# Kernel tuning notes

Hardware: AMD Instinct MI355X
Metric: run time of the kernel (lower is better)

Reference implementation:

```python
import jax, jax.numpy as jnp
import numpy as np

N_HEADS = 16
N_KV_HEADS = 4
HEAD_DIM = 64
ROPE_BASE = 10000.0

def _rope_cos_sin(T, dtype):
    # flash-attn style: cos/sin of shape [T, head_dim//2]
    inv_freq = 1.0 / (ROPE_BASE ** (jnp.arange(0, HEAD_DIM, 2, dtype=jnp.float32) / HEAD_DIM))
    freqs = jnp.arange(T, dtype=jnp.float32)[:, None] * inv_freq[None, :]  # [T, D/2]
    return jnp.cos(freqs).astype(dtype), jnp.sin(freqs).astype(dtype)

def _apply_rope(x, cos, sin):
    # x: [B, H, T, D], non-interleaved rotate-half on full head dim
    d2 = HEAD_DIM // 2
    x1, x2 = x[..., :d2], x[..., d2:]
    c = cos[None, None, :, :]
    s = sin[None, None, :, :]
    return jnp.concatenate([x1 * c - x2 * s, x2 * c + x1 * s], axis=-1)

def setup_inputs() -> dict:
    key = jax.random.key(0)
    ks = jax.random.split(key, 6)
    B, T, D = 1, 4096, 1024
    def g(k, shape, scale):
        return jax.random.normal(k, shape, dtype=jnp.float32) * scale
    return {
        "query": g(ks[0], (B, T, D), 1.0),
        "Wq": g(ks[1], (D, D), D ** -0.5),
        "Wk": g(ks[2], (D, N_KV_HEADS * HEAD_DIM), D ** -0.5),
        "Wv": g(ks[3], (D, N_KV_HEADS * HEAD_DIM), D ** -0.5),
        "W1": g(ks[4], (D, 4 * D), D ** -0.5),
        "W2": g(ks[5], (4 * D, D), (4 * D) ** -0.5),
    }

def reference(query, Wq, Wk, Wv, W1, W2):
    B, T, D = query.shape
    # QKV projections -> [B, H, T, Dh]
    q = (query @ Wq).reshape(B, T, N_HEADS, HEAD_DIM).transpose(0, 2, 1, 3)
    k = (query @ Wk).reshape(B, T, N_KV_HEADS, HEAD_DIM).transpose(0, 2, 1, 3)
    v = (query @ Wv).reshape(B, T, N_KV_HEADS, HEAD_DIM).transpose(0, 2, 1, 3)
    # RoPE (seqlen_offset = 0, no cache)
    cos, sin = _rope_cos_sin(T, q.dtype)
    q = _apply_rope(q, cos, sin)
    k = _apply_rope(k, cos, sin)
    # GQA: repeat KV heads to match Q heads
    n_rep = N_HEADS // N_KV_HEADS
    k = jnp.repeat(k, n_rep, axis=1)
    v = jnp.repeat(v, n_rep, axis=1)
    # Scaled dot-product attention, causal
    scale = HEAD_DIM ** -0.5
    scores = jnp.einsum("bhqd,bhkd->bhqk", q, k) * scale
    i = jnp.arange(T)[:, None]
    j = jnp.arange(T)[None, :]
    scores = jnp.where(j > i, jnp.finfo(scores.dtype).min, scores)
    attn = jax.nn.softmax(scores, axis=-1)
    out = jnp.einsum("bhqk,bhkd->bhqd", attn, v)  # [B, H, T, Dh]
    out = out.transpose(0, 2, 1, 3).reshape(B, T, D)
    # out_proj: Linear -> SiLU -> Linear (use_swiglu=True path)
    return jax.nn.silu(out @ W1) @ W2
```

## Files before the change

### kernel.cpp

```cpp
#include <hip/hip_runtime.h>
#include <stdint.h>

typedef unsigned short u16;
typedef __bf16 bf16x8 __attribute__((ext_vector_type(8)));
typedef float f32x4 __attribute__((ext_vector_type(4)));

#define T_SEQ 4096
#define DMODEL 1024

__device__ __forceinline__ float bf2f(u16 x) {
  union { uint32_t u; float f; } v; v.u = ((uint32_t)x) << 16; return v.f;
}
__device__ __forceinline__ u16 f2bf(float f) {
  union { float f; uint32_t u; } v; v.f = f;
  return (u16)((v.u + 0x7FFFu + ((v.u >> 16) & 1u)) >> 16);
}
__device__ __forceinline__ float fexp2(float x) {
#if __has_builtin(__builtin_amdgcn_exp2f)
  return __builtin_amdgcn_exp2f(x);
#else
  return __expf(x * 0.6931471805599453f);
#endif
}
__device__ __forceinline__ uint32_t pack_bf16(float lo, float hi) {
#if __has_builtin(__builtin_amdgcn_cvt_pk_bf16_f32)
  typedef __bf16 bf16x2_t __attribute__((ext_vector_type(2)));
  union { bf16x2_t v; uint32_t u; } c;
  c.v = __builtin_amdgcn_cvt_pk_bf16_f32(lo, hi);
  return c.u;
#else
  union { float f; uint32_t u; } a, b;
  a.f = lo; b.f = hi;
  return __builtin_amdgcn_perm(b.u + 0x8000u, a.u + 0x8000u, 0x07060302u);
#endif
}
__device__ __forceinline__ void async16(void* lds, const void* g) {
  __builtin_amdgcn_global_load_lds(
      (__attribute__((address_space(1))) void*)const_cast<void*>(g),
      (__attribute__((address_space(3))) void*)lds, 16, 0, 0);
}
__device__ __forceinline__ void storeC(u16* C, size_t i, float v) { C[i] = f2bf(v); }
__device__ __forceinline__ void storeC(float* C, size_t i, float v) { C[i] = v; }

__device__ __forceinline__ void wtrans_body(const float* __restrict__ in,
                                            u16* __restrict__ out, int K, int N,
                                            int bx, int by, int tid,
                                            float (*tile)[65]) {
  const int n0 = bx * 64, k0 = by * 64;
  const int r = tid >> 2, c = (tid & 3) * 16;
#pragma unroll
  for (int j = 0; j < 4; ++j) {
    float4 v = *(const float4*)&in[(size_t)(k0 + r) * N + n0 + c + j * 4];
    tile[r][c + j * 4 + 0] = v.x; tile[r][c + j * 4 + 1] = v.y;
    tile[r][c + j * 4 + 2] = v.z; tile[r][c + j * 4 + 3] = v.w;
  }
  __syncthreads();
  union { u16 s[16]; uint4 q[2]; } buf;
#pragma unroll
  for (int j = 0; j < 16; ++j) buf.s[j] = f2bf(tile[c + j][r]);
  u16* dst = out + (size_t)(n0 + r) * K + k0 + c;
  *(uint4*)(dst) = buf.q[0];
  *(uint4*)(dst + 8) = buf.q[1];
}

__global__ void __launch_bounds__(256) prep(const float* __restrict__ query,
                                            const float* __restrict__ Wq,
                                            const float* __restrict__ Wk,
                                            const float* __restrict__ Wv,
                                            const float* __restrict__ W1,
                                            const float* __restrict__ W2,
                                            u16* __restrict__ Xb,
                                            u16* __restrict__ WqkvT,
                                            u16* __restrict__ W1T,
                                            u16* __restrict__ W2T) {
  __shared__ float tile[64][65];
  const int b = blockIdx.x, tid = threadIdx.x;
  if (b < 4096) {
    int idx = (b * 256 + tid) * 4;
    float4 v = *(const float4*)(query + idx);
    union { u16 s[4]; uint2 q; } o;
    o.s[0] = f2bf(v.x); o.s[1] = f2bf(v.y); o.s[2] = f2bf(v.z); o.s[3] = f2bf(v.w);
    *(uint2*)(Xb + idx) = o.q;
  } else if (b < 4352) {
    int t = b - 4096;
    wtrans_body(Wq, WqkvT, 1024, 1024, t & 15, t >> 4, tid, tile);
  } else if (b < 4416) {
    int t = b - 4352;
    wtrans_body(Wk, WqkvT + (size_t)1024 * 1024, 1024, 256, t & 3, t >> 2, tid, tile);
  } else if (b < 4480) {
    int t = b - 4416;
    wtrans_body(Wv, WqkvT + (size_t)1280 * 1024, 1024, 256, t & 3, t >> 2, tid, tile);
  } else if (b < 5504) {
    int t = b - 4480;
    wtrans_body(W1, W1T, 1024, 4096, t & 63, t >> 6, tid, tile);
  } else {
    int t = b - 5504;
    wtrans_body(W2, W2T, 4096, 1024, t & 15, t >> 4, tid, tile);
  }
}

__global__ void __launch_bounds__(256) rope_vt(const u16* __restrict__ qkv,
                                               u16* __restrict__ Q,
                                               u16* __restrict__ Ko,
                                               u16* __restrict__ Vt) {
  __shared__ u16 tile[64][65];
  const int b = blockIdx.x, tid = threadIdx.x;
  if (b < 4096) {
    const int t = b;
    const int i = tid & 31;
    const float ang = (float)t * powf(10000.f, -(float)i * (1.f / 32.f));
    float s, c;
    sincosf(ang, &s, &c);
    const u16* row = qkv + (size_t)t * 1536;
    const float QS = 0.125f * 1.4426950408889634f;
    const float cq = c * QS, sq = s * QS;
#pragma unroll
    for (int it = 0; it < 2; ++it) {
      int h = (tid >> 5) + it * 8;
      float x1 = bf2f(row[h * 64 + i]);
      float x2 = bf2f(row[h * 64 + 32 + i]);
      size_t o = ((size_t)h * T_SEQ + t) * 64 + i;
      Q[o] = f2bf(x1 * cq - x2 * sq);
      Q[o + 32] = f2bf(x2 * cq + x1 * sq);
    }
    if (tid < 128) {
      int h = tid >> 5;
      float x1 = bf2f(row[1024 + h * 64 + i]);
      float x2 = bf2f(row[1024 + h * 64 + 32 + i]);
      size_t o = ((size_t)h * T_SEQ + t) * 64 + i;
      Ko[o] = f2bf(x1 * c - x2 * s);
      Ko[o + 32] = f2bf(x2 * c + x1 * s);
    }
  } else {
    const int t = b - 4096;
    const int t0 = (t & 63) * 64, h = t >> 6;
    const int r = tid >> 2, q4 = (tid & 3) * 16;
    const u16* src = qkv + (size_t)(t0 + r) * 1536 + 1280 + h * 64 + q4;
    union { u16 s[16]; uint4 q[2]; } buf;
    buf.q[0] = *(const uint4*)(src);
    buf.q[1] = *(const uint4*)(src + 8);
#pragma unroll
    for (int j = 0; j < 16; ++j) tile[r][q4 + j] = buf.s[j];
    __syncthreads();
#pragma unroll
    for (int j = 0; j < 16; ++j) buf.s[j] = tile[q4 + j][r];
    u16* dst = Vt + ((size_t)h * 64 + r) * T_SEQ + t0 + q4;
    *(uint4*)(dst) = buf.q[0];
    *(uint4*)(dst + 8) = buf.q[1];
  }
}

template <int AM, int ACT, typename OutT>
__global__ void __launch_bounds__(256) gemm_bt(const u16* __restrict__ A,
                                               const u16* __restrict__ Bt,
                                               OutT* __restrict__ C,
                                               int M, int N, int K) {
  __shared__ u16 sA[2][AM * 32][64];
  __shared__ u16 sB[2][128][64];
  const int tid = threadIdx.x;
  const int w = tid >> 6, lane = tid & 63;
  const int g = lane >> 4, l15 = lane & 15;
  const int r8 = lane >> 3, c8 = lane & 7;
  const int bm = blockIdx.y * (AM * 32), bn = blockIdx.x * 128;

  f32x4 acc[AM][4];
#pragma unroll
  for (int i = 0; i < AM; ++i)
#pragma unroll
    for (int j = 0; j < 4; ++j) acc[i][j] = (f32x4){0.f, 0.f, 0.f, 0.f};

  const u16* Ag = A + (size_t)(bm + w * (AM * 8) + r8) * K + (c8 ^ r8) * 8;
  const u16* Bg = Bt + (size_t)(bn + w * 32 + r8) * K + (c8 ^ r8) * 8;
  const int mrow = (w >> 1) * (AM * 16), ncol = (w & 1) * 64;
  const int swz = l15 & 7;

#define GSTAGE(K0, BUF)                                                        \
  {                                                                            \
    _Pragma("unroll") for (int t = 0; t < AM; ++t)                             \
      async16(&sA[BUF][w * (AM * 8) + t * 8][0], Ag + (size_t)(t * 8) * K + (K0)); \
    _Pragma("unroll") for (int t = 0; t < 4; ++t)                              \
      async16(&sB[BUF][w * 32 + t * 8][0], Bg + (size_t)(t * 8) * K + (K0));   \
  }

  GSTAGE(0, 0);
  int cur = 0;
  for (int k0 = 0; k0 < K; k0 += 64) {
    __syncthreads();
    if (k0 + 64 < K) GSTAGE(k0 + 64, cur ^ 1);
#pragma unroll
    for (int kk = 0; kk < 2; ++kk) {
      const int cb = ((kk * 4 + g) ^ swz) * 8;
      bf16x8 a[AM], b[4];
#pragma unroll
      for (int i = 0; i < AM; ++i) a[i] = *(const bf16x8*)&sA[cur][mrow + i * 16 + l15][cb];
#pragma unroll
      for (int i = 0; i < 4; ++i) b[i] = *(const bf16x8*)&sB[cur][ncol + i * 16 + l15][cb];
#pragma unroll
      for (int mi = 0; mi < AM; ++mi)
#pragma unroll
        for (int ni = 0; ni < 4; ++ni)
          acc[mi][ni] = __builtin_amdgcn_mfma_f32_16x16x32_bf16(a[mi], b[ni], acc[mi][ni], 0, 0, 0);
    }
    cur ^= 1;
  }
#undef GSTAGE
#pragma unroll
  for (int mi = 0; mi < AM; ++mi)
#pragma unroll
    for (int ni = 0; ni < 4; ++ni)
#pragma unroll
      for (int r = 0; r < 4; ++r) {
        int row = bm + mrow + mi * 16 + g * 4 + r;
        int col = bn + ncol + ni * 16 + l15;
        float v = acc[mi][ni][r];
        if (ACT == 1) v = v / (1.f + __expf(-v));
        storeC(C, (size_t)row * N + col, v);
      }
}

__global__ void __launch_bounds__(512, 2) gemm_ffn1(const u16* __restrict__ A,
                                                    const u16* __restrict__ Bt,
                                                    u16* __restrict__ C) {
  const int N = 4096, K = 1024;
  __shared__ u16 sA[2][256][64];
  __shared__ u16 sB[2][256][64];
  const int tid = threadIdx.x;
  const int w = tid >> 6, lane = tid & 63;
  const int g = lane >> 4, l15 = lane & 15;
  const int r8 = lane >> 3, c8 = lane & 7;
  const int wm = w >> 2, wn = w & 3;
  const int bm = blockIdx.y * 256, bn = blockIdx.x * 256;

  f32x4 acc[8][4];
#pragma unroll
  for (int i = 0; i < 8; ++i)
#pragma unroll
    for (int j = 0; j < 4; ++j) acc[i][j] = (f32x4){0.f, 0.f, 0.f, 0.f};

  const u16* Ag = A + (size_t)(bm + w * 32 + r8) * K + (c8 ^ r8) * 8;
  const u16* Bg = Bt + (size_t)(bn + w * 32 + r8) * K + (c8 ^ r8) * 8;
  const int mrow = wm * 128, ncol = wn * 64;
  const int swz = l15 & 7;

#define FSTAGE(K0, BUF)                                                   \
  {                                                                       \
    _Pragma("unroll") for (int t = 0; t < 4; ++t) {                       \
      async16(&sA[BUF][w * 32 + t * 8][0], Ag + (size_t)(t * 8) * K + (K0)); \
      async16(&sB[BUF][w * 32 + t * 8][0], Bg + (size_t)(t * 8) * K + (K0)); \
    }                                                                     \
  }

  FSTAGE(0, 0);
  int cur = 0;
  for (int k0 = 0; k0 < K; k0 += 64) {
    __syncthreads();
    if (k0 + 64 < K) FSTAGE(k0 + 64, cur ^ 1);
#pragma unroll
    for (int kk = 0; kk < 2; ++kk) {
      const int cb = ((kk * 4 + g) ^ swz) * 8;
      bf16x8 a[8], b[4];
#pragma unroll
      for (int i = 0; i < 8; ++i) a[i] = *(const bf16x8*)&sA[cur][mrow + i * 16 + l15][cb];
#pragma unroll
      for (int i = 0; i < 4; ++i) b[i] = *(const bf16x8*)&sB[cur][ncol + i * 16 + l15][cb];
#pragma unroll
      for (int mi = 0; mi < 8; ++mi)
#pragma unroll
        for (int ni = 0; ni < 4; ++ni)
          acc[mi][ni] = __builtin_amdgcn_mfma_f32_16x16x32_bf16(a[mi], b[ni], acc[mi][ni], 0, 0, 0);
    }
    cur ^= 1;
  }
#undef FSTAGE
#pragma unroll
  for (int mi = 0; mi < 8; ++mi)
#pragma unroll
    for (int ni = 0; ni < 4; ++ni)
#pragma unroll
      for (int r = 0; r < 4; ++r) {
        int row = bm + mrow + mi * 16 + g * 4 + r;
        int col = bn + ncol + ni * 16 + l15;
        float v = acc[mi][ni][r];
        v = v / (1.f + __expf(-v));
        C[(size_t)row * N + col] = f2bf(v);
      }
}

__global__ void __launch_bounds__(512, 2) gemm_w2(const u16* __restrict__ A,
                                                  const u16* __restrict__ Bt,
                                                  float* __restrict__ C0,
                                                  u16* __restrict__ C1) {
  __shared__ u16 sA[2][256][64];
  __shared__ u16 sB[2][128][64];
  const int K = 4096, N = 1024;
  const int z = blockIdx.z, koff = z * 2048;
  const int tid = threadIdx.x;
  const int w = tid >> 6, lane = tid & 63;
  const int g = lane >> 4, l15 = lane & 15;
  const int r8 = lane >> 3, c8 = lane & 7;
  const int wm = w >> 1, wn = w & 1;
  const int bm = blockIdx.y * 256, bn = blockIdx.x * 128;

  f32x4 acc[4][4];
#pragma unroll
  for (int i = 0; i < 4; ++i)
#pragma unroll
    for (int j = 0; j < 4; ++j) acc[i][j] = (f32x4){0.f, 0.f, 0.f, 0.f};

  const u16* Ag = A + (size_t)(bm + w * 32 + r8) * K + koff + (c8 ^ r8) * 8;
  const u16* Bg = Bt + (size_t)(bn + w * 16 + r8) * K + koff + (c8 ^ r8) * 8;
  const int mrow = wm * 64, ncol = wn * 64;
  const int swz = l15 & 7;

#define GSTAGE(K0, BUF)                                                   \
  {                                                                       \
    _Pragma("unroll") for (int t = 0; t < 4; ++t)                         \
      async16(&sA[BUF][w * 32 + t * 8][0], Ag + (size_t)(t * 8) * K + (K0)); \
    _Pragma("unroll") for (int t = 0; t < 2; ++t)                         \
      async16(&sB[BUF][w * 16 + t * 8][0], Bg + (size_t)(t * 8) * K + (K0)); \
  }

  GSTAGE(0, 0);
  int cur = 0;
  for (int k0 = 0; k0 < 2048; k0 += 64) {
    __syncthreads();
    if (k0 + 64 < 2048) GSTAGE(k0 + 64, cur ^ 1);
#pragma unroll
    for (int kk = 0; kk < 2; ++kk) {
      const int cb = ((kk * 4 + g) ^ swz) * 8;
      bf16x8 a[4], b[4];
#pragma unroll
      for (int i = 0; i < 4; ++i) {
        a[i] = *(const bf16x8*)&sA[cur][mrow + i * 16 + l15][cb];
        b[i] = *(const bf16x8*)&sB[cur][ncol + i * 16 + l15][cb];
      }
#pragma unroll
      for (int mi = 0; mi < 4; ++mi)
#pragma unroll
        for (int ni = 0; ni < 4; ++ni)
          acc[mi][ni] = __builtin_amdgcn_mfma_f32_16x16x32_bf16(a[mi], b[ni], acc[mi][ni], 0, 0, 0);
    }
    cur ^= 1;
  }
#undef GSTAGE
#pragma unroll
  for (int mi = 0; mi < 4; ++mi)
#pragma unroll
    for (int ni = 0; ni < 4; ++ni)
#pragma unroll
      for (int r = 0; r < 4; ++r) {
        size_t idx = (size_t)(bm + mrow + mi * 16 + g * 4 + r) * N + bn + ncol + ni * 16 + l15;
        if (z == 0) C0[idx] = acc[mi][ni][r];
        else        C1[idx] = f2bf(acc[mi][ni][r]);
      }
}

__global__ void __launch_bounds__(256) w2_combine(float* __restrict__ out,
                                                  const u16* __restrict__ P1) {
  int idx = (blockIdx.x * 256 + threadIdx.x) * 4;
  float4 v = *(const float4*)(out + idx);
  union { uint2 q; u16 s[4]; } p;
  p.q = *(const uint2*)(P1 + idx);
  v.x += bf2f(p.s[0]); v.y += bf2f(p.s[1]);
  v.z += bf2f(p.s[2]); v.w += bf2f(p.s[3]);
  *(float4*)(out + idx) = v;
}

__global__ void __launch_bounds__(256, 2) attn(const u16* __restrict__ Q,
                                               const u16* __restrict__ K,
                                               const u16* __restrict__ Vt,
                                               u16* __restrict__ O0,
                                               u16* __restrict__ O1,
                                               float* __restrict__ L0,
                                               float* __restrict__ L1) {
  __shared__ u16 sK[2][64][64];
  __shared__ u16 sV[2][64][64];
  __shared__ u16 sP[4][64][68];
  const int pr = blockIdx.x >> 1;
  const int split = blockIdx.x & 1;
  const int h = blockIdx.y;
  const int kvh = h >> 2;
  const int tid = threadIdx.x;
  const int w = tid >> 6, lane = tid & 63;
  const int g = lane >> 4, l15 = lane & 15;
  const int r8 = lane >> 3, c8 = lane & 7;
  const int swz = l15 & 7;
  const int t0 = pr, t1 = 31 - pr;
  const int off = split * 64;

  u16* Op = split ? O1 : O0;
  float* Lp = split ? L1 : L0;

  bf16x8 qf[2][2][2];
  {
    const u16* Qh = Q + (size_t)h * T_SEQ * 64;
#pragma unroll
    for (int half = 0; half < 2; ++half)
#pragma unroll
      for (int mi = 0; mi < 2; ++mi) {
        const int q = (half ? t1 : t0) * 128 + w * 32 + mi * 16 + l15;
#pragma unroll
        for (int kk = 0; kk < 2; ++kk)
          qf[half][mi][kk] = *(const bf16x8*)(Qh + (size_t)q * 64 + (kk * 4 + g) * 8);
      }
  }

  f32x4 oacc[2][2][4];
  f32x4 lacc[2][2];
#pragma unroll
  for (int half = 0; half < 2; ++half)
#pragma unroll
    for (int mi = 0; mi < 2; ++mi) {
      lacc[half][mi] = (f32x4){0.f, 0.f, 0.f, 0.f};
#pragma unroll
      for (int nd = 0; nd < 4; ++nd) oacc[half][mi][nd] = (f32x4){0.f, 0.f, 0.f, 0.f};
    }

  bf16x8 ONES;
  {
    union { u16 s[8]; bf16x8 v; } o;
#pragma unroll
    for (int i = 0; i < 8; ++i) o.s[i] = 0x3F80;
    ONES = o.v;
  }

  const u16* Kg = K + ((size_t)kvh * T_SEQ + w * 16 + r8) * 64 + (c8 ^ r8) * 8;
  const u16* Vg = Vt + ((size_t)kvh * 64 + w * 16 + r8) * T_SEQ + (c8 ^ r8) * 8;

#define STAGE(J, B)                                                     \
  {                                                                     \
    const int kv0_ = (J) * 64;                                          \
    async16(&sK[B][w * 16 + 0][0], Kg + (size_t)kv0_ * 64);             \
    async16(&sK[B][w * 16 + 8][0], Kg + (size_t)(kv0_ + 8) * 64);       \
    async16(&sV[B][w * 16 + 0][0], Vg + kv0_);                          \
    async16(&sV[B][w * 16 + 8][0], Vg + (size_t)8 * T_SEQ + kv0_);      \
  }

#define BODY(B, ACT0, M0, M1)                                                     \
  {                                                                               \
    const int b_ = (B);                                                           \
    f32x4 s1[2][4], s0[2][4];                                                     \
    _Pragma("unroll") for (int mi = 0; mi < 2; ++mi)                              \
    _Pragma("unroll") for (int kt = 0; kt < 4; ++kt) {                            \
      s1[mi][kt] = (f32x4){0.f, 0.f, 0.f, 0.f};                                   \
      if (ACT0) s0[mi][kt] = (f32x4){0.f, 0.f, 0.f, 0.f};                         \
    }                                                                             \
    __builtin_amdgcn_s_setprio(1);                                                \
    _Pragma("unroll") for (int kt = 0; kt < 4; ++kt)                              \
    _Pragma("unroll") for (int kk = 0; kk < 2; ++kk) {                            \
      bf16x8 kf = *(const bf16x8*)&sK[b_][kt * 16 + l15][((kk * 4 + g) ^ swz) * 8]; \
      _Pragma("unroll") for (int mi = 0; mi < 2; ++mi) {                          \
        s1[mi][kt] = __builtin_amdgcn_mfma_f32_16x16x32_bf16(kf, qf[1][mi][kk], s1[mi][kt], 0, 0, 0); \
        if (ACT0)                                                                 \
          s0[mi][kt] = __builtin_amdgcn_mfma_f32_16x16x32_bf16(kf, qf[0][mi][kk], s0[mi][kt], 0, 0, 0); \
      }                                                                           \
    }                                                                             \
    __builtin_amdgcn_s_setprio(0);                                                \
    _Pragma("unroll") for (int mi = 0; mi < 2; ++mi) {                            \
      const int thr_ = w * 32 + mi * 16 + l15 - off;                              \
      _Pragma("unroll") for (int kt = 0; kt < 4; ++kt) {                          \
        float p_[4];                                                              \
        _Pragma("unroll") for (int r = 0; r < 4; ++r) {                           \
          float p = fexp2(s1[mi][kt][r]);                                         \
          if (M1 && (kt * 16 + g * 4 + r > thr_)) p = 0.f;                        \
          p_[r] = p;                                                              \
        }                                                                         \
        uint2 pk;                                                                 \
        pk.x = pack_bf16(p_[0], p_[1]);                                           \
        pk.y = pack_bf16(p_[2], p_[3]);                                           \
        *(uint2*)&sP[w][32 + mi * 16 + l15][kt * 16 + g * 4] = pk;                \
      }                                                                           \
      if (ACT0) {                                                                 \
        _Pragma("unroll") for (int kt = 0; kt < 4; ++kt) {                        \
          float p_[4];                                                            \
          _Pragma("unroll") for (int r = 0; r < 4; ++r) {                         \
            float p = fexp2(s0[mi][kt][r]);                                       \
            if (M0 && (kt * 16 + g * 4 + r > thr_)) p = 0.f;                      \
            p_[r] = p;                                                            \
          }                                                                       \
          uint2 pk;                                                               \
          pk.x = pack_bf16(p_[0], p_[1]);                                         \
          pk.y = pack_bf16(p_[2], p_[3]);                                         \
          *(uint2*)&sP[w][mi * 16 + l15][kt * 16 + g * 4] = pk;                   \
        }                                                                         \
      }                                                                           \
    }                                                                             \
    __builtin_amdgcn_wave_barrier();          \
    __builtin_amdgcn_s_setprio(1);                                                \
    _Pragma("unroll") for (int kk = 0; kk < 2; ++kk) {                            \
      bf16x8 pf1[2], pf0[2];                                                      \
      _Pragma("unroll") for (int mi = 0; mi < 2; ++mi) {                          \
        pf1[mi] = *(const bf16x8*)&sP[w][32 + mi * 16 + l15][kk * 32 + g * 8];    \
        if (ACT0) pf0[mi] = *(const bf16x8*)&sP[w][mi * 16 + l15][kk * 32 + g * 8]; \
      }                                                                           \
      _Pragma("unroll") for (int mi = 0; mi < 2; ++mi) {                          \
        lacc[1][mi] = __builtin_amdgcn_mfma_f32_16x16x32_bf16(pf1[mi], ONES, lacc[1][mi], 0, 0, 0); \
        if (ACT0)                                                                 \
          lacc[0][mi] = __builtin_amdgcn_mfma_f32_16x16x32_bf16(pf0[mi], ONES, lacc[0][mi], 0, 0, 0); \
      }                                                                           \
      _Pragma("unroll") for (int nd = 0; nd < 4; ++nd) {                          \
        bf16x8 vf = *(const bf16x8*)&sV[b_][nd * 16 + l15][((kk * 4 + g) ^ swz) * 8]; \
        _Pragma("unroll") for (int mi = 0; mi < 2; ++mi) {                        \
          oacc[1][mi][nd] = __builtin_amdgcn_mfma_f32_16x16x32_bf16(pf1[mi], vf, oacc[1][mi][nd], 0, 0, 0); \
          if (ACT0)                                                               \
            oacc[0][mi][nd] = __builtin_amdgcn_mfma_f32_16x16x32_bf16(pf0[mi], vf, oacc[0][mi][nd], 0, 0, 0); \
        }                                                                         \
      }                                                                           \
    }                                                                             \
    __builtin_amdgcn_s_setprio(0);                                                \
  }

  const int e0 = 2 * t0 + split, e1 = 2 * t1 + split;
  STAGE(split, 0);
  int jj = split, b = 0;
  for (; jj < e0; jj += 2, b ^= 1) {
    __syncthreads();
    STAGE(jj + 2, b ^ 1);
    BODY(b, true, false, false);
  }
  {
    __syncthreads();
    STAGE(jj + 2, b ^ 1);
    BODY(b, true, true, false);
    jj += 2; b ^= 1;
  }
  for (; jj < e1; jj += 2, b ^= 1) {
    __syncthreads();
    STAGE(jj + 2, b ^ 1);
    BODY(b, false, false, false);
  }
  {
    __syncthreads();
    BODY(b, false, false, true);
  }
#undef STAGE
#undef BODY

#pragma unroll
  for (int half = 0; half < 2; ++half) {
    const int tb = (half ? t1 : t0) * 128;
#pragma unroll
    for (int mi = 0; mi < 2; ++mi)
#pragma unroll
      for (int r = 0; r < 4; ++r) {
        const int trow = tb + w * 32 + mi * 16 + g * 4 + r;
#pragma unroll
        for (int nd = 0; nd < 4; ++nd)
          Op[(size_t)trow * DMODEL + h * 64 + nd * 16 + l15] = f2bf(oacc[half][mi][nd][r]);
        if (l15 == 0) Lp[h * T_SEQ + trow] = lacc[half][mi][r];
      }
  }
}

__global__ void __launch_bounds__(256) attn_combine(const u16* __restrict__ O0,
                                                    const u16* __restrict__ O1,
                                                    const float* __restrict__ L0,
                                                    const float* __restrict__ L1,
                                                    u16* __restrict__ AO) {
  const int t = blockIdx.x, tid = threadIdx.x;
  const int h = tid >> 4, d4 = (tid & 15) * 4;
  const float inv = 1.f / (L0[h * T_SEQ + t] + L1[h * T_SEQ + t]);
  const size_t idx = (size_t)t * DMODEL + h * 64 + d4;
  union { uint2 q; u16 s[4]; } a, b, o;
  a.q = *(const uint2*)(O0 + idx);
  b.q = *(const uint2*)(O1 + idx);
#pragma unroll
  for (int i = 0; i < 4; ++i) o.s[i] = f2bf((bf2f(a.s[i]) + bf2f(b.s[i])) * inv);
  *(uint2*)(AO + idx) = o.q;
}

extern "C" void kernel_launch(void* const* d_in, const int* in_sizes, int n_in,
                              void* d_out, int out_size, void* d_ws, size_t ws_size,
                              hipStream_t stream) {
  const float* query = (const float*)d_in[0];
  const float* Wq = (const float*)d_in[1];
  const float* Wk = (const float*)d_in[2];
  const float* Wv = (const float*)d_in[3];
  const float* W1 = (const float*)d_in[4];
  const float* W2 = (const float*)d_in[5];
  float* out = (float*)d_out;

  char* ws = (char*)d_ws;
  size_t off = 0;
  auto alloc = [&](size_t bytes) { char* p = ws + off; off += (bytes + 255) & ~(size_t)255; return p; };
  u16* Xb   = (u16*)alloc((size_t)4096 * 1024 * 2);
  u16* QKVb = (u16*)alloc((size_t)4096 * 1536 * 2);
  u16* Qb   = (u16*)alloc((size_t)16 * 4096 * 64 * 2);
  u16* Kb   = (u16*)alloc((size_t)4 * 4096 * 64 * 2);
  u16* Vtb  = (u16*)alloc((size_t)4 * 4096 * 64 * 2);
  u16* H    = (u16*)ws;
  u16*   O0p = Xb;
  u16*   O1p = QKVb;
  float* L0p = (float*)(QKVb + (size_t)4096 * 1024);
  float* L1p = L0p + 16 * T_SEQ;
  u16* WqkvT = (u16*)alloc((size_t)1536 * 1024 * 2);
  u16* W1T   = (u16*)alloc((size_t)4096 * 1024 * 2);
  u16* W2T   = (u16*)alloc((size_t)1024 * 4096 * 2);
  u16* AO    = (u16*)alloc((size_t)4096 * 1024 * 2);
  u16* P1    = W1T;
  (void)ws_size; (void)in_sizes; (void)n_in; (void)out_size;

  prep<<<6528, 256, 0, stream>>>(query, Wq, Wk, Wv, W1, W2, Xb, WqkvT, W1T, W2T);
  gemm_bt<2, 0, u16><<<dim3(12, 64), 256, 0, stream>>>(Xb, WqkvT, QKVb, 4096, 1536, 1024);
  rope_vt<<<4352, 256, 0, stream>>>(QKVb, Qb, Kb, Vtb);
  attn<<<dim3(32, 16), 256, 0, stream>>>(Qb, Kb, Vtb, O0p, O1p, L0p, L1p);
  attn_combine<<<4096, 256, 0, stream>>>(O0p, O1p, L0p, L1p, AO);
  gemm_ffn1<<<dim3(16, 16), 512, 0, stream>>>(AO, W1T, H);
  gemm_w2<<<dim3(8, 16, 2), 512, 0, stream>>>(H, W2T, out, P1);
  w2_combine<<<4096, 256, 0, stream>>>(out, P1);
}
```

Before: 284.1 us.

## Fuse RoPE into QKV GEMM epilogue, precompute cos/sin table, retile W2 GEMM

The RoPE rotation for Q and K now runs in the QKV GEMM epilogue, using a cos/sin table computed in the prep kernel, instead of in a separate pass that re-read QKV from memory. The rope_vt kernel is reduced to the V transpose, which removes a read and write of Q/K and the per-token sincos work. Separately, the W2 GEMM uses 256-thread blocks with a 128x128 tile and twice as many blocks, which changes occupancy and tile reuse. The fused epilogue writes 2-byte scattered stores per lane, which may coalesce poorly.

```diff
diff --git a/kernel.cpp b/kernel.cpp
--- a/kernel.cpp
+++ b/kernel.cpp
@@ -39,8 +39,6 @@
       (__attribute__((address_space(1))) void*)const_cast<void*>(g),
       (__attribute__((address_space(3))) void*)lds, 16, 0, 0);
 }
-__device__ __forceinline__ void storeC(u16* C, size_t i, float v) { C[i] = f2bf(v); }
-__device__ __forceinline__ void storeC(float* C, size_t i, float v) { C[i] = v; }
 
 __device__ __forceinline__ void wtrans_body(const float* __restrict__ in,
                                             u16* __restrict__ out, int K, int N,
@@ -72,7 +70,8 @@
                                             u16* __restrict__ Xb,
                                             u16* __restrict__ WqkvT,
                                             u16* __restrict__ W1T,
-                                            u16* __restrict__ W2T) {
+                                            u16* __restrict__ W2T,
+                                            float2* __restrict__ CS) {
   __shared__ float tile[64][65];
   const int b = blockIdx.x, tid = threadIdx.x;
   if (b < 4096) {
@@ -93,91 +92,69 @@
   } else if (b < 5504) {
     int t = b - 4480;
     wtrans_body(W1, W1T, 1024, 4096, t & 63, t >> 6, tid, tile);
-  } else {
+  } else if (b < 6528) {
     int t = b - 5504;
     wtrans_body(W2, W2T, 4096, 1024, t & 15, t >> 4, tid, tile);
+  } else {
+    int idx = (b - 6528) * 256 + tid;
+    int t = idx >> 5, i = idx & 31;
+    float ang = (float)t * powf(10000.f, -(float)i * (1.f / 32.f));
+    float s, c;
+    sincosf(ang, &s, &c);
+    CS[idx] = make_float2(c, s);
   }
 }
 
 __global__ void __launch_bounds__(256) rope_vt(const u16* __restrict__ qkv,
-                                               u16* __restrict__ Q,
-                                               u16* __restrict__ Ko,
                                                u16* __restrict__ Vt) {
   __shared__ u16 tile[64][65];
   const int b = blockIdx.x, tid = threadIdx.x;
-  if (b < 4096) {
-    const int t = b;
-    const int i = tid & 31;
-    const float ang = (float)t * powf(10000.f, -(float)i * (1.f / 32.f));
-    float s, c;
-    sincosf(ang, &s, &c);
-    const u16* row = qkv + (size_t)t * 1536;
-    const float QS = 0.125f * 1.4426950408889634f;
-    const float cq = c * QS, sq = s * QS;
-#pragma unroll
-    for (int it = 0; it < 2; ++it) {
-      int h = (tid >> 5) + it * 8;
-      float x1 = bf2f(row[h * 64 + i]);
-      float x2 = bf2f(row[h * 64 + 32 + i]);
-      size_t o = ((size_t)h * T_SEQ + t) * 64 + i;
-      Q[o] = f2bf(x1 * cq - x2 * sq);
-      Q[o + 32] = f2bf(x2 * cq + x1 * sq);
-    }
-    if (tid < 128) {
-      int h = tid >> 5;
-      float x1 = bf2f(row[1024 + h * 64 + i]);
-      float x2 = bf2f(row[1024 + h * 64 + 32 + i]);
-      size_t o = ((size_t)h * T_SEQ + t) * 64 + i;
-      Ko[o] = f2bf(x1 * c - x2 * s);
-      Ko[o + 32] = f2bf(x2 * c + x1 * s);
-    }
-  } else {
-    const int t = b - 4096;
-    const int t0 = (t & 63) * 64, h = t >> 6;
-    const int r = tid >> 2, q4 = (tid & 3) * 16;
-    const u16* src = qkv + (size_t)(t0 + r) * 1536 + 1280 + h * 64 + q4;
-    union { u16 s[16]; uint4 q[2]; } buf;
-    buf.q[0] = *(const uint4*)(src);
-    buf.q[1] = *(const uint4*)(src + 8);
-#pragma unroll
-    for (int j = 0; j < 16; ++j) tile[r][q4 + j] = buf.s[j];
-    __syncthreads();
-#pragma unroll
-    for (int j = 0; j < 16; ++j) buf.s[j] = tile[q4 + j][r];
-    u16* dst = Vt + ((size_t)h * 64 + r) * T_SEQ + t0 + q4;
-    *(uint4*)(dst) = buf.q[0];
-    *(uint4*)(dst + 8) = buf.q[1];
-  }
-}
-
-template <int AM, int ACT, typename OutT>
-__global__ void __launch_bounds__(256) gemm_bt(const u16* __restrict__ A,
-                                               const u16* __restrict__ Bt,
-                                               OutT* __restrict__ C,
-                                               int M, int N, int K) {
-  __shared__ u16 sA[2][AM * 32][64];
+  const int t0 = (b & 63) * 64, h = b >> 6;
+  const int r = tid >> 2, q4 = (tid & 3) * 16;
+  const u16* src = qkv + (size_t)(t0 + r) * 1536 + 1280 + h * 64 + q4;
+  union { u16 s[16]; uint4 q[2]; } buf;
+  buf.q[0] = *(const uint4*)(src);
+  buf.q[1] = *(const uint4*)(src + 8);
+#pragma unroll
+  for (int j = 0; j < 16; ++j) tile[r][q4 + j] = buf.s[j];
+  __syncthreads();
+#pragma unroll
+  for (int j = 0; j < 16; ++j) buf.s[j] = tile[q4 + j][r];
+  u16* dst = Vt + ((size_t)h * 64 + r) * T_SEQ + t0 + q4;
+  *(uint4*)(dst) = buf.q[0];
+  *(uint4*)(dst + 8) = buf.q[1];
+}
+
+__global__ void __launch_bounds__(256) gemm_qkv(const u16* __restrict__ A,
+                                                const u16* __restrict__ Bt,
+                                                const float2* __restrict__ CS,
+                                                u16* __restrict__ Qo,
+                                                u16* __restrict__ Ko,
+                                                u16* __restrict__ QKVb) {
+  const int N = 1536, K = 1024;
+  __shared__ u16 sA[2][64][64];
   __shared__ u16 sB[2][128][64];
   const int tid = threadIdx.x;
   const int w = tid >> 6, lane = tid & 63;
   const int g = lane >> 4, l15 = lane & 15;
   const int r8 = lane >> 3, c8 = lane & 7;
-  const int bm = blockIdx.y * (AM * 32), bn = blockIdx.x * 128;
-
-  f32x4 acc[AM][4];
-#pragma unroll
-  for (int i = 0; i < AM; ++i)
+  const int bm = blockIdx.y * 64, bn = blockIdx.x * 128;
+
+  f32x4 acc[2][4];
+#pragma unroll
+  for (int i = 0; i < 2; ++i)
 #pragma unroll
     for (int j = 0; j < 4; ++j) acc[i][j] = (f32x4){0.f, 0.f, 0.f, 0.f};
 
-  const u16* Ag = A + (size_t)(bm + w * (AM * 8) + r8) * K + (c8 ^ r8) * 8;
+  const u16* Ag = A + (size_t)(bm + w * 16 + r8) * K + (c8 ^ r8) * 8;
   const u16* Bg = Bt + (size_t)(bn + w * 32 + r8) * K + (c8 ^ r8) * 8;
-  const int mrow = (w >> 1) * (AM * 16), ncol = (w & 1) * 64;
+  const int mrow = (w >> 1) * 32, ncol = (w & 1) * 64;
   const int swz = l15 & 7;
 
 #define GSTAGE(K0, BUF)                                                        \
   {                                                                            \
-    _Pragma("unroll") for (int t = 0; t < AM; ++t)                             \
-      async16(&sA[BUF][w * (AM * 8) + t * 8][0], Ag + (size_t)(t * 8) * K + (K0)); \
+    _Pragma("unroll") for (int t = 0; t < 2; ++t)                              \
+      async16(&sA[BUF][w * 16 + t * 8][0], Ag + (size_t)(t * 8) * K + (K0));   \
     _Pragma("unroll") for (int t = 0; t < 4; ++t)                              \
       async16(&sB[BUF][w * 32 + t * 8][0], Bg + (size_t)(t * 8) * K + (K0));   \
   }
@@ -190,13 +167,13 @@
 #pragma unroll
     for (int kk = 0; kk < 2; ++kk) {
       const int cb = ((kk * 4 + g) ^ swz) * 8;
-      bf16x8 a[AM], b[4];
-#pragma unroll
-      for (int i = 0; i < AM; ++i) a[i] = *(const bf16x8*)&sA[cur][mrow + i * 16 + l15][cb];
+      bf16x8 a[2], b[4];
+#pragma unroll
+      for (int i = 0; i < 2; ++i) a[i] = *(const bf16x8*)&sA[cur][mrow + i * 16 + l15][cb];
 #pragma unroll
       for (int i = 0; i < 4; ++i) b[i] = *(const bf16x8*)&sB[cur][ncol + i * 16 + l15][cb];
 #pragma unroll
-      for (int mi = 0; mi < AM; ++mi)
+      for (int mi = 0; mi < 2; ++mi)
 #pragma unroll
         for (int ni = 0; ni < 4; ++ni)
           acc[mi][ni] = __builtin_amdgcn_mfma_f32_16x16x32_bf16(a[mi], b[ni], acc[mi][ni], 0, 0, 0);
@@ -204,18 +181,53 @@
     cur ^= 1;
   }
 #undef GSTAGE
-#pragma unroll
-  for (int mi = 0; mi < AM; ++mi)
-#pragma unroll
-    for (int ni = 0; ni < 4; ++ni)
+
+  const int col0 = bn + ncol;
+  const int head = col0 >> 6;
+  if (head < 16) {
+    const float QS = 0.125f * 1.4426950408889634f;
+#pragma unroll
+    for (int mi = 0; mi < 2; ++mi)
 #pragma unroll
       for (int r = 0; r < 4; ++r) {
-        int row = bm + mrow + mi * 16 + g * 4 + r;
-        int col = bn + ncol + ni * 16 + l15;
-        float v = acc[mi][ni][r];
-        if (ACT == 1) v = v / (1.f + __expf(-v));
-        storeC(C, (size_t)row * N + col, v);
+        const int t = bm + mrow + mi * 16 + g * 4 + r;
+        u16* Qrow = Qo + ((size_t)head * T_SEQ + t) * 64;
+#pragma unroll
+        for (int ni = 0; ni < 2; ++ni) {
+          float2 cs = CS[t * 32 + ni * 16 + l15];
+          float x1 = acc[mi][ni][r], x2 = acc[mi][ni + 2][r];
+          Qrow[ni * 16 + l15]      = f2bf((x1 * cs.x - x2 * cs.y) * QS);
+          Qrow[32 + ni * 16 + l15] = f2bf((x2 * cs.x + x1 * cs.y) * QS);
+        }
       }
+  } else if (head < 20) {
+    const int kvh = head - 16;
+#pragma unroll
+    for (int mi = 0; mi < 2; ++mi)
+#pragma unroll
+      for (int r = 0; r < 4; ++r) {
+        const int t = bm + mrow + mi * 16 + g * 4 + r;
+        u16* Krow = Ko + ((size_t)kvh * T_SEQ + t) * 64;
+#pragma unroll
+        for (int ni = 0; ni < 2; ++ni) {
+          float2 cs = CS[t * 32 + ni * 16 + l15];
+          float x1 = acc[mi][ni][r], x2 = acc[mi][ni + 2][r];
+          Krow[ni * 16 + l15]      = f2bf(x1 * cs.x - x2 * cs.y);
+          Krow[32 + ni * 16 + l15] = f2bf(x2 * cs.x + x1 * cs.y);
+        }
+      }
+  } else {
+#pragma unroll
+    for (int mi = 0; mi < 2; ++mi)
+#pragma unroll
+      for (int ni = 0; ni < 4; ++ni)
+#pragma unroll
+        for (int r = 0; r < 4; ++r) {
+          int row = bm + mrow + mi * 16 + g * 4 + r;
+          int col = col0 + ni * 16 + l15;
+          QKVb[(size_t)row * N + col] = f2bf(acc[mi][ni][r]);
+        }
+  }
 }
 
 __global__ void __launch_bounds__(512, 2) gemm_ffn1(const u16* __restrict__ A,
@@ -286,11 +298,11 @@
       }
 }
 
-__global__ void __launch_bounds__(512, 2) gemm_w2(const u16* __restrict__ A,
+__global__ void __launch_bounds__(256, 2) gemm_w2(const u16* __restrict__ A,
                                                   const u16* __restrict__ Bt,
                                                   float* __restrict__ C0,
                                                   u16* __restrict__ C1) {
-  __shared__ u16 sA[2][256][64];
+  __shared__ u16 sA[2][128][64];
   __shared__ u16 sB[2][128][64];
   const int K = 4096, N = 1024;
   const int z = blockIdx.z, koff = z * 2048;
@@ -298,8 +310,7 @@
   const int w = tid >> 6, lane = tid & 63;
   const int g = lane >> 4, l15 = lane & 15;
   const int r8 = lane >> 3, c8 = lane & 7;
-  const int wm = w >> 1, wn = w & 1;
-  const int bm = blockIdx.y * 256, bn = blockIdx.x * 128;
+  const int bm = blockIdx.y * 128, bn = blockIdx.x * 128;
 
   f32x4 acc[4][4];
 #pragma unroll
@@ -308,16 +319,16 @@
     for (int j = 0; j < 4; ++j) acc[i][j] = (f32x4){0.f, 0.f, 0.f, 0.f};
 
   const u16* Ag = A + (size_t)(bm + w * 32 + r8) * K + koff + (c8 ^ r8) * 8;
-  const u16* Bg = Bt + (size_t)(bn + w * 16 + r8) * K + koff + (c8 ^ r8) * 8;
-  const int mrow = wm * 64, ncol = wn * 64;
+  const u16* Bg = Bt + (size_t)(bn + w * 32 + r8) * K + koff + (c8 ^ r8) * 8;
+  const int mrow = (w >> 1) * 64, ncol = (w & 1) * 64;
   const int swz = l15 & 7;
 
 #define GSTAGE(K0, BUF)                                                   \
   {                                                                       \
-    _Pragma("unroll") for (int t = 0; t < 4; ++t)                         \
+    _Pragma("unroll") for (int t = 0; t < 4; ++t) {                       \
       async16(&sA[BUF][w * 32 + t * 8][0], Ag + (size_t)(t * 8) * K + (K0)); \
-    _Pragma("unroll") for (int t = 0; t < 2; ++t)                         \
-      async16(&sB[BUF][w * 16 + t * 8][0], Bg + (size_t)(t * 8) * K + (K0)); \
+      async16(&sB[BUF][w * 32 + t * 8][0], Bg + (size_t)(t * 8) * K + (K0)); \
+    }                                                                     \
   }
 
   GSTAGE(0, 0);
@@ -597,15 +608,16 @@
   u16* W1T   = (u16*)alloc((size_t)4096 * 1024 * 2);
   u16* W2T   = (u16*)alloc((size_t)1024 * 4096 * 2);
   u16* AO    = (u16*)alloc((size_t)4096 * 1024 * 2);
+  float2* CS = (float2*)alloc((size_t)4096 * 32 * 8);
   u16* P1    = W1T;
   (void)ws_size; (void)in_sizes; (void)n_in; (void)out_size;
 
-  prep<<<6528, 256, 0, stream>>>(query, Wq, Wk, Wv, W1, W2, Xb, WqkvT, W1T, W2T);
-  gemm_bt<2, 0, u16><<<dim3(12, 64), 256, 0, stream>>>(Xb, WqkvT, QKVb, 4096, 1536, 1024);
-  rope_vt<<<4352, 256, 0, stream>>>(QKVb, Qb, Kb, Vtb);
+  prep<<<7040, 256, 0, stream>>>(query, Wq, Wk, Wv, W1, W2, Xb, WqkvT, W1T, W2T, CS);
+  gemm_qkv<<<dim3(12, 64), 256, 0, stream>>>(Xb, WqkvT, CS, Qb, Kb, QKVb);
+  rope_vt<<<256, 256, 0, stream>>>(QKVb, Vtb);
   attn<<<dim3(32, 16), 256, 0, stream>>>(Qb, Kb, Vtb, O0p, O1p, L0p, L1p);
   attn_combine<<<4096, 256, 0, stream>>>(O0p, O1p, L0p, L1p, AO);
   gemm_ffn1<<<dim3(16, 16), 512, 0, stream>>>(AO, W1T, H);
-  gemm_w2<<<dim3(8, 16, 2), 512, 0, stream>>>(H, W2T, out, P1);
+  gemm_w2<<<dim3(8, 32, 2), 256, 0, stream>>>(H, W2T, out, P1);
   w2_combine<<<4096, 256, 0, stream>>>(out, P1);
 }
```

After: 278.5 us. Within noise of the previous version (-2.0%).
